# Kernel tuning notes

Hardware: AMD Instinct MI355X
Metric: run time of the kernel (lower is better)

Reference implementation:

```python
import jax, jax.numpy as jnp
import numpy as np

EPS = 1e-5
NEG = -1e22

def layernorm(x, g, b):
    m = jnp.mean(x, axis=-1, keepdims=True)
    v = jnp.mean((x - m) ** 2, axis=-1, keepdims=True)
    return (x - m) * jax.lax.rsqrt(v + EPS) * g + b

def setup_inputs() -> dict:
    key = jax.random.key(0)
    ks = jax.random.split(key, 16)
    B, N, D, K = 4, 2048, 512, 32
    H = int(D * 1.5)  # 768
    sc = lambda fan_in: 1.0 / np.sqrt(fan_in)
    inp = {
        'x': jax.random.normal(ks[0], (B, N, D), jnp.float32),
        'adj': jax.random.uniform(ks[1], (B, N, N), jnp.float32),
        'inxs': jax.random.randint(ks[2], (B, N, K), 0, N, jnp.int64),
        'Wq': jax.random.normal(ks[3], (D, D), jnp.float32) * sc(D),
        'bq': jnp.zeros((D,), jnp.float32),
        'Wk': jax.random.normal(ks[4], (D, D), jnp.float32) * sc(D),
        'bk': jnp.zeros((D,), jnp.float32),
        'Wv': jax.random.normal(ks[5], (D, D), jnp.float32) * sc(D),
        'bv': jnp.zeros((D,), jnp.float32),
        'Wo': jax.random.normal(ks[6], (D, D), jnp.float32) * sc(D),
        'bo': jnp.zeros((D,), jnp.float32),
        'g1': jnp.ones((D,), jnp.float32),
        'beta1': jnp.zeros((D,), jnp.float32),
        'W1': jax.random.normal(ks[7], (D, H), jnp.float32) * sc(D),
        'bf1': jnp.zeros((H,), jnp.float32),
        'W2': jax.random.normal(ks[8], (H, D), jnp.float32) * sc(H),
        'bf2': jnp.zeros((D,), jnp.float32),
        'g2': jnp.ones((D,), jnp.float32),
        'beta2': jnp.zeros((D,), jnp.float32),
    }
    return inp

def reference(x, adj, inxs, Wq, bq, Wk, bk, Wv, bv, Wo, bo, g1, beta1, W1, bf1, W2, bf2, g2, beta2):
    B, N, D = x.shape
    # projections
    q = x @ Wq + bq                                   # [B,N,D]
    k = x @ Wk + bk
    v = x @ Wv + bv
    # gather top-k neighbor keys/values: [B,N,K,D]
    b_idx = jnp.arange(B)[:, None, None]
    k_nei = k[b_idx, inxs]
    v_nei = v[b_idx, inxs]
    # attention over selected neighbors, masked by adjacency sign
    scores = jnp.einsum('bnd,bnkd->bnk', q, k_nei) / jnp.sqrt(jnp.float32(D))
    adj_nei = jnp.take_along_axis(adj, inxs, axis=2)  # [B,N,K]
    mask = jnp.where(adj_nei > 0, 0.0, NEG)
    attn = jax.nn.softmax(scores + mask, axis=-1)
    att_out = jnp.einsum('bnk,bnkd->bnd', attn, v_nei) @ Wo + bo
    # residual + LN
    y = layernorm(x + jax.nn.relu(att_out), g1, beta1)
    # FFN + residual + LN
    h = jax.nn.relu(y @ W1 + bf1) @ W2 + bf2
    return layernorm(y + h, g2, beta2)
```

## Files before the change

kernel.cpp:

```cpp
#include <hip/hip_runtime.h>
#include <stdint.h>

typedef __attribute__((ext_vector_type(8))) short short8;
typedef __attribute__((ext_vector_type(4))) float f32x4;
typedef __attribute__((ext_vector_type(2))) _Float16 h2;
typedef __attribute__((ext_vector_type(8))) _Float16 half8;

#define QSCALE 21.1666667f
#define VSCALE 0.04724409449f
#define SCONST 9.86413e-5f

static __device__ __forceinline__ unsigned short f2bf(float f) {
  unsigned int u = __float_as_uint(f);
  u += 0x7FFFu + ((u >> 16) & 1u);
  return (unsigned short)(u >> 16);
}
static __device__ __forceinline__ float bf2f(unsigned short h) {
  return __uint_as_float(((unsigned int)h) << 16);
}
static __device__ __forceinline__ unsigned short f2h(float f) {
  _Float16 h = (_Float16)f;
  return __builtin_bit_cast(unsigned short, h);
}
static __device__ __forceinline__ signed char q8(float v) {
  float sv = fminf(fmaxf(v * QSCALE, -127.f), 127.f);
  return (signed char)(int)rintf(sv);
}
static __device__ __forceinline__ unsigned char qu8(float v) {
  return (unsigned char)(int)rintf(fminf(fmaxf(v * QSCALE + 128.f, 0.f), 255.f));
}
static __device__ __forceinline__ float ub(unsigned int x, int n) {
  return (float)((x >> (8 * n)) & 0xffu);
}

#define GLD16(gp, lp) __builtin_amdgcn_global_load_lds( \
    (__attribute__((address_space(1))) void*)(gp), \
    (__attribute__((address_space(3))) void*)(lp), 16, 0, 0)

__global__ __launch_bounds__(256) void k_prep(
    const float* __restrict__ adj, const int* __restrict__ inxs,
    float* __restrict__ maskb, const float* __restrict__ x,
    unsigned short* __restrict__ xb,
    const float* __restrict__ Wq, const float* __restrict__ Wk,
    const float* __restrict__ Wv, const float* __restrict__ Wo,
    const float* __restrict__ W1, const float* __restrict__ W2,
    unsigned short* __restrict__ wqkvt, unsigned short* __restrict__ wot,
    unsigned short* __restrict__ w1t, unsigned short* __restrict__ w2t) {
  __shared__ float tile[32][33];
  const int bid = blockIdx.x;
  const int t = threadIdx.x;
  if (bid < 1024) {
    const int xcd = bid & 7;
    const int bb = xcd >> 1;
    const int s = ((bid >> 3) << 1) | (xcd & 1);
    const long row = ((long)bb << 11) | ((long)s << 3) | (t >> 5);
    const int kk = t & 31;
    const int idx = inxs[row * 32 + kk];
    const float a = adj[row * 2048 + idx];
    maskb[row * 32 + kk] = a > 0.f ? 0.f : -1e22f;
    return;
  }
  if (bid < 3072) {
    const int lb = bid - 1024;
    const int xcd = lb & 7;
    const int bb = xcd >> 1;
    const int s = ((lb >> 3) << 1) | (xcd & 1);
    const long row = ((long)bb << 11) | ((long)s << 2) | (t >> 6);
    const int lane = t & 63;
    const float4* p = (const float4*)(x + row * 512 + lane * 8);
    float4 a = p[0], b = p[1];
    short8 v;
    v[0] = (short)f2h(a.x); v[1] = (short)f2h(a.y);
    v[2] = (short)f2h(a.z); v[3] = (short)f2h(a.w);
    v[4] = (short)f2h(b.x); v[5] = (short)f2h(b.y);
    v[6] = (short)f2h(b.z); v[7] = (short)f2h(b.w);
    *(short8*)(xb + row * 512 + lane * 8) = v;
    return;
  }
  const int lb = bid - 3072;
  const float* src;
  unsigned short* dst;
  int R, C, f16, local;
  if (lb < 768) {
    const int m = lb >> 8;
    src = m == 0 ? Wq : (m == 1 ? Wk : Wv);
    dst = wqkvt + (long)m * 512 * 512;
    R = 512; C = 512; f16 = 1; local = lb & 255;
  } else if (lb < 1024) {
    src = Wo; dst = wot; R = 512; C = 512; f16 = 0; local = lb - 768;
  } else if (lb < 1408) {
    src = W1; dst = w1t; R = 512; C = 768; f16 = 0; local = lb - 1024;
  } else {
    src = W2; dst = w2t; R = 768; C = 512; f16 = 0; local = lb - 1408;
  }
  const int ntx = C >> 5;
  const int c0 = (local % ntx) << 5;
  const int r0 = (local / ntx) << 5;
  const int tx = t & 31, ty = t >> 5;
#pragma unroll
  for (int i = 0; i < 4; i++)
    tile[ty + i * 8][tx] = src[(long)(r0 + ty + i * 8) * C + c0 + tx];
  __syncthreads();
#pragma unroll
  for (int i = 0; i < 4; i++) {
    float v = tile[tx][ty + i * 8];
    dst[(long)(c0 + ty + i * 8) * R + r0 + tx] = f16 ? f2h(v) : f2bf(v);
  }
}

__global__ __launch_bounds__(256) void k_gemm_qkv(
    const unsigned short* __restrict__ A, const unsigned short* __restrict__ Bt,
    const float* __restrict__ bq, const float* __restrict__ bk,
    const float* __restrict__ bv, signed char* __restrict__ qk8,
    unsigned char* __restrict__ v8) {
  const int K = 512;
  __shared__ unsigned short As[2][128 * 64];
  __shared__ unsigned short Bs[2][128 * 64];
  const int t = threadIdx.x;
  const int lane = t & 63;
  const int w = t >> 6;
  const int wr = w >> 1, wc = w & 1;
  const int lin = blockIdx.x;
  const int xcd = lin & 7;
  const int bb = xcd >> 1;
  const int s = ((lin >> 3) << 1) | (xcd & 1);
  const int m0 = (bb * 16 + s / 12) * 128;
  const int n0 = (s % 12) * 128;

  f32x4 acc[4][4];
#pragma unroll
  for (int mi = 0; mi < 4; mi++)
#pragma unroll
    for (int ni = 0; ni < 4; ni++) {
      f32x4 z = {0.f, 0.f, 0.f, 0.f};
      acc[mi][ni] = z;
    }

  auto stage = [&](int buf, int k0) {
#pragma unroll
    for (int i = 0; i < 4; i++) {
      const int c = t + i * 256;
      const int r = c >> 3, j = c & 7;
      GLD16(A + (long)(m0 + r) * K + k0 + ((j ^ (r & 7)) << 3), &As[buf][c * 8]);
    }
#pragma unroll
    for (int i = 0; i < 4; i++) {
      const int c = t + i * 256;
      const int r = c >> 3, j = c & 7;
      GLD16(Bt + (long)(n0 + r) * K + k0 + ((j ^ (r & 7)) << 3), &Bs[buf][c * 8]);
    }
  };

  const int nt = K >> 6;
  stage(0, 0);
  for (int tt = 0; tt < nt; ++tt) {
    const int cur = tt & 1;
    if (tt + 1 < nt) {
      stage(cur ^ 1, (tt + 1) << 6);
      asm volatile("s_waitcnt vmcnt(8)" ::: "memory");
    } else {
      asm volatile("s_waitcnt vmcnt(0)" ::: "memory");
    }
    __builtin_amdgcn_s_barrier();

#pragma unroll
    for (int kk = 0; kk < 2; kk++) {
      short8 af[4], bf[4];
#pragma unroll
      for (int mi = 0; mi < 4; mi++) {
        const int r = wr * 64 + mi * 16 + (lane & 15);
        const int jj = (kk << 2) + (lane >> 4);
        af[mi] = *(const short8*)&As[cur][r * 64 + ((jj ^ (r & 7)) << 3)];
      }
#pragma unroll
      for (int ni = 0; ni < 4; ni++) {
        const int r = wc * 64 + ni * 16 + (lane & 15);
        const int jj = (kk << 2) + (lane >> 4);
        bf[ni] = *(const short8*)&Bs[cur][r * 64 + ((jj ^ (r & 7)) << 3)];
      }
#pragma unroll
      for (int mi = 0; mi < 4; mi++)
#pragma unroll
        for (int ni = 0; ni < 4; ni++)
          acc[mi][ni] = __builtin_amdgcn_mfma_f32_16x16x32_f16(
              __builtin_bit_cast(half8, af[mi]), __builtin_bit_cast(half8, bf[ni]),
              acc[mi][ni], 0, 0, 0);
    }
    asm volatile("s_waitcnt lgkmcnt(0)" ::: "memory");
    __builtin_amdgcn_s_barrier();
  }

  const int lr = (lane >> 4) * 4;
  const int lc = lane & 15;
  if (n0 < 1024) {
#pragma unroll
    for (int mi = 0; mi < 4; mi++) {
#pragma unroll
      for (int ni = 0; ni < 4; ni++) {
        const int col = n0 + wc * 64 + ni * 16 + lc;
        const float bvv = col < 512 ? bq[col] : bk[col - 512];
#pragma unroll
        for (int r = 0; r < 4; r++) {
          const int row = m0 + wr * 64 + mi * 16 + lr + r;
          qk8[(long)row * 1024 + col] = q8(acc[mi][ni][r] + bvv);
        }
      }
    }
  } else {
#pragma unroll
    for (int mi = 0; mi < 4; mi++) {
#pragma unroll
      for (int ni = 0; ni < 4; ni++) {
        const int col = n0 + wc * 64 + ni * 16 + lc;
        const float bvv = bv[col - 1024];
#pragma unroll
        for (int r = 0; r < 4; r++) {
          const int row = m0 + wr * 64 + mi * 16 + lr + r;
          v8[(long)row * 512 + (col - 1024)] = qu8(acc[mi][ni][r] + bvv);
        }
      }
    }
  }
}

template <int EPI>
__global__ __launch_bounds__(256) void k_gemm(const unsigned short* __restrict__ A,
                                              const unsigned short* __restrict__ Bt,
                                              const float* __restrict__ bias,
                                              unsigned short* __restrict__ C,
                                              int M, int N, int K) {
  __shared__ unsigned short As[2][128 * 64];
  __shared__ unsigned short Bs[2][64 * 64];
  const int t = threadIdx.x;
  const int lane = t & 63;
  const int w = t >> 6;
  const int wr = w >> 1, wc = w & 1;
  const int lin = blockIdx.x;
  const int xcd = lin & 7;
  const int bb = xcd >> 1;
  const int nx = N >> 6;
  const int s = ((lin >> 3) << 1) | (xcd & 1);
  const int m0 = (bb * 16 + s / nx) * 128;
  const int n0 = (s % nx) * 64;

  f32x4 acc[4][2];
#pragma unroll
  for (int mi = 0; mi < 4; mi++)
#pragma unroll
    for (int ni = 0; ni < 2; ni++) {
      f32x4 z = {0.f, 0.f, 0.f, 0.f};
      acc[mi][ni] = z;
    }

  auto stage = [&](int buf, int k0) {
#pragma unroll
    for (int i = 0; i < 4; i++) {
      const int c = t + i * 256;
      const int r = c >> 3, j = c & 7;
      GLD16(A + (long)(m0 + r) * K + k0 + ((j ^ (r & 7)) << 3), &As[buf][c * 8]);
    }
#pragma unroll
    for (int i = 0; i < 2; i++) {
      const int c = t + i * 256;
      const int r = c >> 3, j = c & 7;
      GLD16(Bt + (long)(n0 + r) * K + k0 + ((j ^ (r & 7)) << 3), &Bs[buf][c * 8]);
    }
  };

  const int nt = K >> 6;
  stage(0, 0);
  for (int tt = 0; tt < nt; ++tt) {
    const int cur = tt & 1;
    if (tt + 1 < nt) {
      stage(cur ^ 1, (tt + 1) << 6);
      asm volatile("s_waitcnt vmcnt(6)" ::: "memory");
    } else {
      asm volatile("s_waitcnt vmcnt(0)" ::: "memory");
    }
    __builtin_amdgcn_s_barrier();

#pragma unroll
    for (int kk = 0; kk < 2; kk++) {
      short8 af[4], bf[2];
#pragma unroll
      for (int mi = 0; mi < 4; mi++) {
        const int r = wr * 64 + mi * 16 + (lane & 15);
        const int jj = (kk << 2) + (lane >> 4);
        af[mi] = *(const short8*)&As[cur][r * 64 + ((jj ^ (r & 7)) << 3)];
      }
#pragma unroll
      for (int ni = 0; ni < 2; ni++) {
        const int r = wc * 32 + ni * 16 + (lane & 15);
        const int jj = (kk << 2) + (lane >> 4);
        bf[ni] = *(const short8*)&Bs[cur][r * 64 + ((jj ^ (r & 7)) << 3)];
      }
#pragma unroll
      for (int mi = 0; mi < 4; mi++)
#pragma unroll
        for (int ni = 0; ni < 2; ni++)
          acc[mi][ni] = __builtin_amdgcn_mfma_f32_16x16x32_bf16(af[mi], bf[ni], acc[mi][ni], 0, 0, 0);
    }
    asm volatile("s_waitcnt lgkmcnt(0)" ::: "memory");
    __builtin_amdgcn_s_barrier();
  }

  const int lr = (lane >> 4) * 4;
  const int lc = lane & 15;
#pragma unroll
  for (int mi = 0; mi < 4; mi++) {
#pragma unroll
    for (int ni = 0; ni < 2; ni++) {
      const int col = n0 + wc * 32 + ni * 16 + lc;
      const float bvv = bias[col];
#pragma unroll
      for (int r = 0; r < 4; r++) {
        const int row = m0 + wr * 64 + mi * 16 + lr + r;
        float v = acc[mi][ni][r] + bvv;
        if (EPI == 1) v = fmaxf(v, 0.f);
        C[(long)row * N + col] = f2bf(v);
      }
    }
  }
}

__global__ __launch_bounds__(256, 8) void k_attn(const signed char* __restrict__ qk8,
                                                 const unsigned char* __restrict__ v8,
                                                 const float* __restrict__ maskb,
                                                 const int* __restrict__ inxs,
                                                 unsigned short* __restrict__ att) {
  const int t = threadIdx.x;
  const int lane = t & 63;
  const int w = t >> 6;
  const int bid = blockIdx.x;
  const int xcd = bid & 7;
  const int b = xcd >> 1;
  const int sub = ((bid >> 3) << 1) | (xcd & 1);
  const int row = (b << 11) | (sub << 2) | w;
  const long base = (long)b * 2048;
  const int g = lane >> 4;
  const int li = lane & 15;
  const int kk = lane & 31;

  const int* ix = inxs + (long)row * 32;
  const int ixv = ix[kk];
  const float mval = maskb[(long)row * 32 + kk];

  const uint2* qp = (const uint2*)(qk8 + (long)row * 1024);
  uint2 qc[4];
#pragma unroll
  for (int c = 0; c < 4; c++) qc[c] = qp[li + c * 16];

  float scr[8];
#pragma unroll
  for (int r = 0; r < 8; r++) {
    const int nb = __shfl(ixv, r * 4 + g, 64);
    const uint2* kp = (const uint2*)(qk8 + (base + nb) * 1024 + 512);
    int di = 0;
#pragma unroll
    for (int c = 0; c < 4; c++) {
      uint2 kc = kp[li + c * 16];
      di = __builtin_amdgcn_sdot4((int)kc.x, (int)qc[c].x, di, false);
      di = __builtin_amdgcn_sdot4((int)kc.y, (int)qc[c].y, di, false);
    }
#pragma unroll
    for (int m = 1; m <= 8; m <<= 1) di += __shfl_xor(di, m, 64);
    scr[r] = (float)di;
  }

  const int srcl = (kk & 3) << 4;
  float s = __shfl(scr[0], srcl, 64);
#pragma unroll
  for (int r = 1; r < 8; r++) {
    const float tr = __shfl(scr[r], srcl, 64);
    s = ((kk >> 2) == r) ? tr : s;
  }
  s = s * SCONST + mval;

  float mx = s;
#pragma unroll
  for (int d = 1; d <= 16; d <<= 1) mx = fmaxf(mx, __shfl_xor(mx, d, 64));
  const float e = __expf(s - mx);
  float ts = e;
#pragma unroll
  for (int d = 1; d <= 16; d <<= 1) ts += __shfl_xor(ts, d, 64);
  const float inv = 1.f / ts;

  float o[8] = {0, 0, 0, 0, 0, 0, 0, 0};
#pragma unroll
  for (int p = 0; p < 32; p++) {
    const int un = __shfl(ixv, p, 64);
    const float wn = __shfl(e, p, 64);
    const uint2 vv = *(const uint2*)(v8 + (base + un) * 512 + lane * 8);
    o[0] += wn * ub(vv.x, 0);
    o[1] += wn * ub(vv.x, 1);
    o[2] += wn * ub(vv.x, 2);
    o[3] += wn * ub(vv.x, 3);
    o[4] += wn * ub(vv.y, 0);
    o[5] += wn * ub(vv.y, 1);
    o[6] += wn * ub(vv.y, 2);
    o[7] += wn * ub(vv.y, 3);
  }

  short8 ov;
#pragma unroll
  for (int j = 0; j < 8; j++)
    ov[j] = (short)f2bf(VSCALE * (o[j] * inv - 128.f));
  *(short8*)(att + (long)row * 512 + lane * 8) = ov;
}

__global__ __launch_bounds__(256) void k_ln1(const float* __restrict__ x,
                                             const unsigned short* __restrict__ o,
                                             const float* __restrict__ g,
                                             const float* __restrict__ beta,
                                             unsigned short* __restrict__ y) {
  const int lane = threadIdx.x & 63;
  const int w = threadIdx.x >> 6;
  const int bid = blockIdx.x;
  const int xcd = bid & 7;
  const int bb = xcd >> 1;
  const int s0 = ((bid >> 3) << 1) | (xcd & 1);
  const long row = ((long)bb << 11) | ((long)s0 << 2) | w;
  const float4* xp = (const float4*)(x + row * 512 + lane * 8);
  float4 x0 = xp[0], x1 = xp[1];
  short8 ov = *(const short8*)(o + row * 512 + lane * 8);
  float tv[8] = {x0.x, x0.y, x0.z, x0.w, x1.x, x1.y, x1.z, x1.w};
  float s = 0.f, s2 = 0.f;
#pragma unroll
  for (int j = 0; j < 8; j++) {
    tv[j] += bf2f((unsigned short)ov[j]);
    s += tv[j];
    s2 += tv[j] * tv[j];
  }
#pragma unroll
  for (int m = 32; m >= 1; m >>= 1) {
    s += __shfl_xor(s, m, 64);
    s2 += __shfl_xor(s2, m, 64);
  }
  const float mean = s * (1.f / 512.f);
  const float var = s2 * (1.f / 512.f) - mean * mean;
  const float r = rsqrtf(var + 1e-5f);
  const float4* gp = (const float4*)(g + lane * 8);
  const float4* bp = (const float4*)(beta + lane * 8);
  float4 g0 = gp[0], g1v = gp[1], b0 = bp[0], b1 = bp[1];
  float gg[8] = {g0.x, g0.y, g0.z, g0.w, g1v.x, g1v.y, g1v.z, g1v.w};
  float bb2[8] = {b0.x, b0.y, b0.z, b0.w, b1.x, b1.y, b1.z, b1.w};
  short8 yv;
#pragma unroll
  for (int j = 0; j < 8; j++) yv[j] = (short)f2bf((tv[j] - mean) * r * gg[j] + bb2[j]);
  *(short8*)(y + row * 512 + lane * 8) = yv;
}

__global__ __launch_bounds__(256) void k_ln2(const unsigned short* __restrict__ y,
                                             const unsigned short* __restrict__ f,
                                             const float* __restrict__ g,
                                             const float* __restrict__ beta,
                                             float* __restrict__ out) {
  const int lane = threadIdx.x & 63;
  const int w = threadIdx.x >> 6;
  const int bid = blockIdx.x;
  const int xcd = bid & 7;
  const int bb = xcd >> 1;
  const int s0 = ((bid >> 3) << 1) | (xcd & 1);
  const long row = ((long)bb << 11) | ((long)s0 << 2) | w;
  short8 yv = *(const short8*)(y + row * 512 + lane * 8);
  short8 fv = *(const short8*)(f + row * 512 + lane * 8);
  float tv[8];
  float s = 0.f, s2 = 0.f;
#pragma unroll
  for (int j = 0; j < 8; j++) {
    tv[j] = bf2f((unsigned short)yv[j]) + bf2f((unsigned short)fv[j]);
    s += tv[j];
    s2 += tv[j] * tv[j];
  }
#pragma unroll
  for (int m = 32; m >= 1; m >>= 1) {
    s += __shfl_xor(s, m, 64);
    s2 += __shfl_xor(s2, m, 64);
  }
  const float mean = s * (1.f / 512.f);
  const float var = s2 * (1.f / 512.f) - mean * mean;
  const float r = rsqrtf(var + 1e-5f);
  const float4* gp = (const float4*)(g + lane * 8);
  const float4* bp = (const float4*)(beta + lane * 8);
  float4 g0 = gp[0], g1v = gp[1], b0 = bp[0], b1 = bp[1];
  float gg[8] = {g0.x, g0.y, g0.z, g0.w, g1v.x, g1v.y, g1v.z, g1v.w};
  float bb2[8] = {b0.x, b0.y, b0.z, b0.w, b1.x, b1.y, b1.z, b1.w};
  float ovv[8];
#pragma unroll
  for (int j = 0; j < 8; j++) ovv[j] = (tv[j] - mean) * r * gg[j] + bb2[j];
  float4* op = (float4*)(out + row * 512 + lane * 8);
  float4 o0 = {ovv[0], ovv[1], ovv[2], ovv[3]};
  float4 o1 = {ovv[4], ovv[5], ovv[6], ovv[7]};
  op[0] = o0;
  op[1] = o1;
}

extern "C" void kernel_launch(void* const* d_in, const int* in_sizes, int n_in,
                              void* d_out, int out_size, void* d_ws, size_t ws_size,
                              hipStream_t stream) {
  const float* x   = (const float*)d_in[0];
  const float* adj = (const float*)d_in[1];
  const int*   inx = (const int*)d_in[2];
  const float* Wq  = (const float*)d_in[3];
  const float* bq  = (const float*)d_in[4];
  const float* Wk  = (const float*)d_in[5];
  const float* bk  = (const float*)d_in[6];
  const float* Wv  = (const float*)d_in[7];
  const float* bv  = (const float*)d_in[8];
  const float* Wo  = (const float*)d_in[9];
  const float* bo  = (const float*)d_in[10];
  const float* g1  = (const float*)d_in[11];
  const float* be1 = (const float*)d_in[12];
  const float* W1  = (const float*)d_in[13];
  const float* bf1 = (const float*)d_in[14];
  const float* W2  = (const float*)d_in[15];
  const float* bf2 = (const float*)d_in[16];
  const float* g2  = (const float*)d_in[17];
  const float* be2 = (const float*)d_in[18];

  unsigned short* xb    = (unsigned short*)d_ws;
  unsigned short* wqkvt = xb + 4194304;
  unsigned short* wot   = wqkvt + 786432;
  unsigned short* w1t   = wot + 262144;
  unsigned short* w2t   = w1t + 393216;
  signed char*    qk8   = (signed char*)(w2t + 393216);
  unsigned char*  v8    = (unsigned char*)(qk8 + 8388608);
  unsigned short* oproj = (unsigned short*)(v8 + 4194304);
  unsigned short* y     = oproj + 4194304;
  float*          maskb = (float*)(y + 4194304);
  unsigned short* att   = xb;
  unsigned short* h     = (unsigned short*)qk8;
  unsigned short* f     = oproj;

  k_prep<<<4864, 256, 0, stream>>>(adj, inx, maskb, x, xb, Wq, Wk, Wv, Wo, W1, W2,
                                   wqkvt, wot, w1t, w2t);
  k_gemm_qkv<<<768, 256, 0, stream>>>(xb, wqkvt, bq, bk, bv, qk8, v8);
  k_attn<<<2048, 256, 0, stream>>>(qk8, v8, maskb, inx, att);
  k_gemm<1><<<512, 256, 0, stream>>>(att, wot, bo, oproj, 8192, 512, 512);
  k_ln1<<<2048, 256, 0, stream>>>(x, oproj, g1, be1, y);
  k_gemm<1><<<768, 256, 0, stream>>>(y, w1t, bf1, h, 8192, 768, 512);
  k_gemm<0><<<512, 256, 0, stream>>>(h, w2t, bf2, f, 8192, 512, 768);
  k_ln2<<<2048, 256, 0, stream>>>(y, f, g2, be2, (float*)d_out);
}
```

Measured before the change: 104.0 us.

## Move mask and weight transposes into QKV GEMM launch; widen attention score loads

The adjacency mask gather and the Wo/W1/W2 transpose-casts leave the prep kernel. They become extra tail blocks of the QKV GEMM kernel, reusing its shared memory as the transpose tile. This shrinks the work that must finish before the QKV GEMM starts and lets that independent work fill the GEMM's tail wave. The extra blocks inherit the GEMM kernel's large LDS footprint, which limits how many run at once. Separately, the attention score dot product now reads q and k as 16-byte chunks instead of 8-byte chunks, halving the number of load instructions per neighbor.

Result: faster. 100.4 us (-3.4%).

```diff
diff --git a/kernel.cpp b/kernel.cpp
--- a/kernel.cpp
+++ b/kernel.cpp
@@ -3,7 +3,6 @@
 
 typedef __attribute__((ext_vector_type(8))) short short8;
 typedef __attribute__((ext_vector_type(4))) float f32x4;
-typedef __attribute__((ext_vector_type(2))) _Float16 h2;
 typedef __attribute__((ext_vector_type(8))) _Float16 half8;
 
 #define QSCALE 21.1666667f
@@ -38,33 +37,16 @@
     (__attribute__((address_space(3))) void*)(lp), 16, 0, 0)
 
 __global__ __launch_bounds__(256) void k_prep(
-    const float* __restrict__ adj, const int* __restrict__ inxs,
-    float* __restrict__ maskb, const float* __restrict__ x,
-    unsigned short* __restrict__ xb,
+    const float* __restrict__ x, unsigned short* __restrict__ xb,
     const float* __restrict__ Wq, const float* __restrict__ Wk,
-    const float* __restrict__ Wv, const float* __restrict__ Wo,
-    const float* __restrict__ W1, const float* __restrict__ W2,
-    unsigned short* __restrict__ wqkvt, unsigned short* __restrict__ wot,
-    unsigned short* __restrict__ w1t, unsigned short* __restrict__ w2t) {
+    const float* __restrict__ Wv, unsigned short* __restrict__ wqkvt) {
   __shared__ float tile[32][33];
   const int bid = blockIdx.x;
   const int t = threadIdx.x;
-  if (bid < 1024) {
+  if (bid < 2048) {
     const int xcd = bid & 7;
     const int bb = xcd >> 1;
     const int s = ((bid >> 3) << 1) | (xcd & 1);
-    const long row = ((long)bb << 11) | ((long)s << 3) | (t >> 5);
-    const int kk = t & 31;
-    const int idx = inxs[row * 32 + kk];
-    const float a = adj[row * 2048 + idx];
-    maskb[row * 32 + kk] = a > 0.f ? 0.f : -1e22f;
-    return;
-  }
-  if (bid < 3072) {
-    const int lb = bid - 1024;
-    const int xcd = lb & 7;
-    const int bb = xcd >> 1;
-    const int s = ((lb >> 3) << 1) | (xcd & 1);
     const long row = ((long)bb << 11) | ((long)s << 2) | (t >> 6);
     const int lane = t & 63;
     const float4* p = (const float4*)(x + row * 512 + lane * 8);
@@ -77,53 +59,80 @@
     *(short8*)(xb + row * 512 + lane * 8) = v;
     return;
   }
-  const int lb = bid - 3072;
-  const float* src;
-  unsigned short* dst;
-  int R, C, f16, local;
-  if (lb < 768) {
-    const int m = lb >> 8;
-    src = m == 0 ? Wq : (m == 1 ? Wk : Wv);
-    dst = wqkvt + (long)m * 512 * 512;
-    R = 512; C = 512; f16 = 1; local = lb & 255;
-  } else if (lb < 1024) {
-    src = Wo; dst = wot; R = 512; C = 512; f16 = 0; local = lb - 768;
-  } else if (lb < 1408) {
-    src = W1; dst = w1t; R = 512; C = 768; f16 = 0; local = lb - 1024;
-  } else {
-    src = W2; dst = w2t; R = 768; C = 512; f16 = 0; local = lb - 1408;
-  }
-  const int ntx = C >> 5;
-  const int c0 = (local % ntx) << 5;
-  const int r0 = (local / ntx) << 5;
+  const int lb = bid - 2048;
+  const int m = lb >> 8;
+  const float* src = m == 0 ? Wq : (m == 1 ? Wk : Wv);
+  unsigned short* dst = wqkvt + (long)m * 512 * 512;
+  const int local = lb & 255;
+  const int c0 = (local & 15) << 5;
+  const int r0 = (local >> 4) << 5;
   const int tx = t & 31, ty = t >> 5;
 #pragma unroll
   for (int i = 0; i < 4; i++)
-    tile[ty + i * 8][tx] = src[(long)(r0 + ty + i * 8) * C + c0 + tx];
+    tile[ty + i * 8][tx] = src[(long)(r0 + ty + i * 8) * 512 + c0 + tx];
   __syncthreads();
 #pragma unroll
-  for (int i = 0; i < 4; i++) {
-    float v = tile[tx][ty + i * 8];
-    dst[(long)(c0 + ty + i * 8) * R + r0 + tx] = f16 ? f2h(v) : f2bf(v);
-  }
-}
-
-__global__ __launch_bounds__(256) void k_gemm_qkv(
+  for (int i = 0; i < 4; i++)
+    dst[(long)(c0 + ty + i * 8) * 512 + r0 + tx] = f2h(tile[tx][ty + i * 8]);
+}
+
+__global__ __launch_bounds__(256) void k_g1x(
     const unsigned short* __restrict__ A, const unsigned short* __restrict__ Bt,
     const float* __restrict__ bq, const float* __restrict__ bk,
     const float* __restrict__ bv, signed char* __restrict__ qk8,
-    unsigned char* __restrict__ v8) {
+    unsigned char* __restrict__ v8,
+    const float* __restrict__ adj, const int* __restrict__ inxs,
+    float* __restrict__ maskb,
+    const float* __restrict__ Wo, const float* __restrict__ W1,
+    const float* __restrict__ W2, unsigned short* __restrict__ wot,
+    unsigned short* __restrict__ w1t, unsigned short* __restrict__ w2t) {
   const int K = 512;
   __shared__ unsigned short As[2][128 * 64];
   __shared__ unsigned short Bs[2][128 * 64];
   const int t = threadIdx.x;
+  const int bid = blockIdx.x;
+
+  if (bid >= 768) {
+    const int eb = bid - 768;
+    if (eb < 1024) {
+      const int xcd = eb & 7;
+      const int bb = xcd >> 1;
+      const int s = ((eb >> 3) << 1) | (xcd & 1);
+      const long row = ((long)bb << 11) | ((long)s << 3) | (t >> 5);
+      const int kk = t & 31;
+      const int idx = inxs[row * 32 + kk];
+      const float a = adj[row * 2048 + idx];
+      maskb[row * 32 + kk] = a > 0.f ? 0.f : -1e22f;
+      return;
+    }
+    float(*tile)[33] = (float(*)[33]) & As[0][0];
+    const int lb = eb - 1024;
+    const float* src;
+    unsigned short* dst;
+    int R, C, local;
+    if (lb < 256) { src = Wo; dst = wot; R = 512; C = 512; local = lb; }
+    else if (lb < 640) { src = W1; dst = w1t; R = 512; C = 768; local = lb - 256; }
+    else { src = W2; dst = w2t; R = 768; C = 512; local = lb - 640; }
+    const int ntx = C >> 5;
+    const int c0 = (local % ntx) << 5;
+    const int r0 = (local / ntx) << 5;
+    const int tx = t & 31, ty = t >> 5;
+#pragma unroll
+    for (int i = 0; i < 4; i++)
+      tile[ty + i * 8][tx] = src[(long)(r0 + ty + i * 8) * C + c0 + tx];
+    __syncthreads();
+#pragma unroll
+    for (int i = 0; i < 4; i++)
+      dst[(long)(c0 + ty + i * 8) * R + r0 + tx] = f2bf(tile[tx][ty + i * 8]);
+    return;
+  }
+
   const int lane = t & 63;
   const int w = t >> 6;
   const int wr = w >> 1, wc = w & 1;
-  const int lin = blockIdx.x;
-  const int xcd = lin & 7;
+  const int xcd = bid & 7;
   const int bb = xcd >> 1;
-  const int s = ((lin >> 3) << 1) | (xcd & 1);
+  const int s = ((bid >> 3) << 1) | (xcd & 1);
   const int m0 = (bb * 16 + s / 12) * 128;
   const int n0 = (s % 12) * 128;
 
@@ -345,22 +354,24 @@
   const int ixv = ix[kk];
   const float mval = maskb[(long)row * 32 + kk];
 
-  const uint2* qp = (const uint2*)(qk8 + (long)row * 1024);
-  uint2 qc[4];
-#pragma unroll
-  for (int c = 0; c < 4; c++) qc[c] = qp[li + c * 16];
+  const uint4* qp = (const uint4*)(qk8 + (long)row * 1024);
+  uint4 qc[2];
+#pragma unroll
+  for (int c = 0; c < 2; c++) qc[c] = qp[li + c * 16];
 
   float scr[8];
 #pragma unroll
   for (int r = 0; r < 8; r++) {
     const int nb = __shfl(ixv, r * 4 + g, 64);
-    const uint2* kp = (const uint2*)(qk8 + (base + nb) * 1024 + 512);
+    const uint4* kp = (const uint4*)(qk8 + (base + nb) * 1024 + 512);
     int di = 0;
 #pragma unroll
-    for (int c = 0; c < 4; c++) {
-      uint2 kc = kp[li + c * 16];
+    for (int c = 0; c < 2; c++) {
+      const uint4 kc = kp[li + c * 16];
       di = __builtin_amdgcn_sdot4((int)kc.x, (int)qc[c].x, di, false);
       di = __builtin_amdgcn_sdot4((int)kc.y, (int)qc[c].y, di, false);
+      di = __builtin_amdgcn_sdot4((int)kc.z, (int)qc[c].z, di, false);
+      di = __builtin_amdgcn_sdot4((int)kc.w, (int)qc[c].w, di, false);
     }
 #pragma unroll
     for (int m = 1; m <= 8; m <<= 1) di += __shfl_xor(di, m, 64);
@@ -532,9 +543,9 @@
   unsigned short* h     = (unsigned short*)qk8;
   unsigned short* f     = oproj;
 
-  k_prep<<<4864, 256, 0, stream>>>(adj, inx, maskb, x, xb, Wq, Wk, Wv, Wo, W1, W2,
-                                   wqkvt, wot, w1t, w2t);
-  k_gemm_qkv<<<768, 256, 0, stream>>>(xb, wqkvt, bq, bk, bv, qk8, v8);
+  k_prep<<<2816, 256, 0, stream>>>(x, xb, Wq, Wk, Wv, wqkvt);
+  k_g1x<<<2816, 256, 0, stream>>>(xb, wqkvt, bq, bk, bv, qk8, v8,
+                                  adj, inx, maskb, Wo, W1, W2, wot, w1t, w2t);
   k_attn<<<2048, 256, 0, stream>>>(qk8, v8, maskb, inx, att);
   k_gemm<1><<<512, 256, 0, stream>>>(att, wot, bo, oproj, 8192, 512, 512);
   k_ln1<<<2048, 256, 0, stream>>>(x, oproj, g1, be1, y);
```
